# Optimization experiments

Hardware: AMD Instinct MI355X
Metric: run time of the kernel (lower is better)

Reference implementation:

```python
import jax, jax.numpy as jnp
import numpy as np

N = 51200      # total nodes
G = 256        # graphs in batch
NPG = 200      # nodes per graph
E = 409600     # intra-graph edges
EPG = E // G
F_IN, HID, HEADS, NCLS = 768, 128, 4, 2


def setup_inputs() -> dict:
    key = jax.random.key(0)
    ks = jax.random.split(key, 20)
    x = jax.random.normal(ks[0], (N, F_IN), jnp.float32)
    # edges strictly inside each graph, no self-loops (PyG batching semantics)
    gid = jnp.arange(E, dtype=jnp.int32) // EPG
    sl = jax.random.randint(ks[1], (E,), 0, NPG, dtype=jnp.int32)
    off = jax.random.randint(ks[2], (E,), 1, NPG, dtype=jnp.int32)
    dl = (sl + off) % NPG
    edge_index = jnp.stack([gid * NPG + sl, gid * NPG + dl])
    batch = jnp.arange(N, dtype=jnp.int32) // NPG

    def glorot(k, shape, fan_in):
        return jax.random.normal(k, shape, jnp.float32) * np.float32(1.0 / np.sqrt(fan_in))

    return {
        'x': x, 'edge_index': edge_index, 'batch': batch,
        'W1': glorot(ks[3], (F_IN, HEADS * HID), F_IN),
        'a_src1': glorot(ks[4], (HEADS, HID), HID),
        'a_dst1': glorot(ks[5], (HEADS, HID), HID),
        'b1': jnp.zeros((HEADS * HID,), jnp.float32),
        'W2': glorot(ks[6], (HEADS * HID, HID), HEADS * HID),
        'a_src2': glorot(ks[7], (1, HID), HID),
        'a_dst2': glorot(ks[8], (1, HID), HID),
        'b2': jnp.zeros((HID,), jnp.float32),
        'Wc': glorot(ks[9], (HID, 2), HID),
        'bc': jnp.zeros((2,), jnp.float32),
        'Wf1': glorot(ks[10], (HID, HID), HID),
        'bf1': jnp.zeros((HID,), jnp.float32),
        'Wf2': glorot(ks[11], (HID, NCLS), HID),
        'bf2': jnp.zeros((NCLS,), jnp.float32),
    }


def _segment_softmax(logits, seg, num):
    m = jax.ops.segment_max(logits, seg, num_segments=num)
    e = jnp.exp(logits - m[seg])
    s = jax.ops.segment_sum(e, seg, num_segments=num)
    return e / (s[seg] + 1e-16)


def _gat(x, src, dst, W, a_s, a_d, b, n):
    # PyG GATConv, eval mode (attention dropout off), self-loops already in src/dst
    H, C = a_s.shape
    h = (x @ W).reshape(n, H, C)                       # [n,H,C]
    a_src = (h * a_s).sum(-1)                          # [n,H]
    a_dst = (h * a_d).sum(-1)
    logits = jax.nn.leaky_relu(a_src[src] + a_dst[dst], 0.2)  # [Etot,H]
    alpha = _segment_softmax(logits, dst, n)
    out = jax.ops.segment_sum(h[src] * alpha[:, :, None], dst, num_segments=n)
    return out.reshape(n, H * C) + b


def reference(x, edge_index, batch, W1, a_src1, a_dst1, b1, W2, a_src2, a_dst2, b2,
              Wc, bc, Wf1, bf1, Wf2, bf2):
    src0, dst0 = edge_index[0], edge_index[1]
    loop = jnp.arange(N, dtype=src0.dtype)
    src = jnp.concatenate([src0, loop])
    dst = jnp.concatenate([dst0, loop])

    h1 = jax.nn.relu(_gat(x, src, dst, W1, a_src1, a_dst1, b1, N))     # [N,512]
    h2 = jax.nn.relu(_gat(h1, src, dst, W2, a_src2, a_dst2, b2, N))    # [N,128]

    S = jax.nn.softmax(h2 @ Wc + bc, axis=1)                           # [N,2]

    # aggregate(): per-graph S^T A S via per-edge outer products (A from original edges)
    eg = batch[src0]
    outer = S[src0][:, :, None] * S[dst0][:, None, :]                  # [E,2,2]
    agg = jax.ops.segment_sum(outer, eg, num_segments=G)               # [G,2,2]
    rnorm = jnp.clip(jnp.abs(agg).sum(axis=2, keepdims=True), 1e-5, None)  # F.normalize p=1 dim=1
    nadj = agg / rnorm
    diag = jnp.diagonal(nadj, axis1=1, axis2=2)                        # [G,2]
    aggregate_loss = jnp.mean(jnp.mean((diag - 1.0) ** 2, axis=1))     # MSE vs ones, averaged over graphs

    # subgraph embedding: first row of S_g^T x_g per graph
    sub = jax.ops.segment_sum(S[:, 0:1] * h2, batch, num_segments=G)   # [G,128]

    out = jax.nn.relu(sub @ Wf1 + bf1)                                 # eval: dropout off
    out = out @ Wf2 + bf2                                              # [G,2]
    return out, aggregate_loss
```

## Files before the change

kernel.cpp:

```cpp
#include <hip/hip_runtime.h>
#include <hip/hip_bf16.h>
#include <cstdint>

#define N_NODES 51200
#define N_GRAPH 256
#define NPG     200
#define N_EDGE  409600
#define EPG     1600
#define F_IN    768
#define HID     128
#define HEADS   4
#define HC      512

typedef __attribute__((ext_vector_type(8))) short short8;
typedef __attribute__((ext_vector_type(4))) float floatx4;

constexpr size_t OFF_H1B    = 0;
constexpr size_t OFF_H2B    = OFF_H1B + (size_t)N_NODES * HC * 2;
constexpr size_t OFF_H2F    = OFF_H2B + (size_t)N_NODES * HID * 2;
constexpr size_t OFF_WT1    = OFF_H2F + (size_t)N_NODES * HID * 4;
constexpr size_t OFF_WT2    = OFF_WT1 + (size_t)HC * F_IN * 2;
constexpr size_t OFF_S      = OFF_WT2 + (size_t)HID * HC * 2;
constexpr size_t OFF_AGG    = OFF_S + (size_t)N_NODES * 2 * 4;
constexpr size_t OFF_SUB    = OFF_AGG + (size_t)N_GRAPH * 4 * 4;

__device__ __forceinline__ float leaky(float x) { return x >= 0.0f ? x : 0.2f * x; }

__device__ __forceinline__ unsigned short f2bf(float f) {
    unsigned int u = __float_as_uint(f);
    u += 0x7fffu + ((u >> 16) & 1u);
    return (unsigned short)(u >> 16);
}
__device__ __forceinline__ float bflo(int p) { return __uint_as_float((unsigned)p << 16); }
__device__ __forceinline__ float bfhi(int p) { return __uint_as_float((unsigned)p & 0xffff0000u); }

__device__ __forceinline__ unsigned int cvtpk(float lo, float hi) {
    unsigned int r;
    asm("v_cvt_pk_bf16_f32 %0, %1, %2" : "=v"(r) : "v"(lo), "v"(hi));
    return r;
}

__device__ __forceinline__ void gl_lds16(const void* g, void* l) {
    __builtin_amdgcn_global_load_lds(
        (__attribute__((address_space(1))) void*)(g),
        (__attribute__((address_space(3))) void*)(l),
        16, 0, 0);
}

__global__ __launch_bounds__(256)
void transpose_cvt_kernel(const float* __restrict__ W, short* __restrict__ Wt,
                          int K, int Nn)
{
    int idx = blockIdx.x * 256 + threadIdx.x;
    if (idx >= K * Nn) return;
    int k = idx / Nn, n = idx % Nn;
    Wt[(size_t)n * K + k] = (short)f2bf(W[idx]);
}

__global__ __launch_bounds__(256, 3)
void gemm_xw1_kernel(const float* __restrict__ A, const short* __restrict__ Bt,
                     unsigned short* __restrict__ C, int M, int Nn, int K)
{
    __shared__ __align__(16) float Asm[2][128 * 32];
    __shared__ __align__(16) short Bsm[2][4096];
    const int tid = threadIdx.x;
    const int w = tid >> 6, l = tid & 63;

    const int nwg = gridDim.x;
    int wg = blockIdx.x;
    wg = (wg & 7) * (nwg >> 3) + (wg >> 3);
    const int nbx = Nn >> 7;
    const int m0 = (wg / nbx) * 128;
    const int n0 = (wg % nbx) * 128;
    const int wr = w >> 1, wc = w & 1;

    floatx4 acc[4][4];
#pragma unroll
    for (int i = 0; i < 4; ++i)
#pragma unroll
        for (int j = 0; j < 4; ++j) acc[i][j] = (floatx4)0.0f;

    const short* bgp = Bt + (size_t)(n0 + w * 32 + (l & 15)) * K + ((l >> 4) * 8);
    const float* agp = A + (size_t)(m0 + w * 32 + (l & 7)) * K + ((l >> 3) * 4);
    const int nt = K >> 5;

    int aB[4];
#pragma unroll
    for (int mi = 0; mi < 4; ++mi)
        aB[mi] = (wr * 8 + mi * 2 + ((l & 15) >> 3)) * 256 + (l >> 4) * 64 + (l & 7) * 4;
    const int bB0 = wc * 2048 + l * 8;

#define STAGE1(buf, t) {                                                        \
        const int ko_ = (t) * 32;                                               \
        gl_lds16(agp + ko_,              &Asm[buf][w * 1024]);                  \
        gl_lds16(agp + 8 * K + ko_,      &Asm[buf][w * 1024 + 256]);            \
        gl_lds16(agp + 16 * K + ko_,     &Asm[buf][w * 1024 + 512]);            \
        gl_lds16(agp + 24 * K + ko_,     &Asm[buf][w * 1024 + 768]);            \
        gl_lds16(bgp + ko_,              &Bsm[buf][w * 1024]);                  \
        gl_lds16(bgp + 16 * K + ko_,     &Bsm[buf][w * 1024 + 512]); }

#define COMPUTE1(buf) {                                                         \
        short8 af[4], bfr[4];                                                   \
        _Pragma("unroll")                                                       \
        for (int mi = 0; mi < 4; ++mi) {                                        \
            float4 v0 = *(const float4*)&Asm[buf][aB[mi]];                      \
            float4 v1 = *(const float4*)&Asm[buf][aB[mi] + 32];                 \
            uint4 pk;                                                           \
            pk.x = cvtpk(v0.x, v0.y); pk.y = cvtpk(v0.z, v0.w);                 \
            pk.z = cvtpk(v1.x, v1.y); pk.w = cvtpk(v1.z, v1.w);                 \
            af[mi] = *reinterpret_cast<short8*>(&pk);                           \
        }                                                                       \
        _Pragma("unroll")                                                       \
        for (int ni = 0; ni < 4; ++ni)                                          \
            bfr[ni] = *(const short8*)&Bsm[buf][bB0 + ni * 512];                \
        _Pragma("unroll")                                                       \
        for (int mi = 0; mi < 4; ++mi)                                          \
            _Pragma("unroll")                                                   \
            for (int ni = 0; ni < 4; ++ni)                                      \
                acc[mi][ni] = __builtin_amdgcn_mfma_f32_16x16x32_bf16(          \
                    af[mi], bfr[ni], acc[mi][ni], 0, 0, 0); }

    STAGE1(0, 0);
    asm volatile("s_waitcnt vmcnt(0)" ::: "memory");
    __builtin_amdgcn_s_barrier();

    int cur = 0;
    for (int t = 0; t < nt; ++t) {
        if (t + 1 < nt) STAGE1(cur ^ 1, t + 1);
        COMPUTE1(cur);
        if (t + 1 < nt) {
            asm volatile("s_waitcnt vmcnt(0) lgkmcnt(0)" ::: "memory");
            __builtin_amdgcn_s_barrier();
            cur ^= 1;
        }
    }
#undef STAGE1
#undef COMPUTE1

    const int lr = (l >> 4) * 4, lc = l & 15;
#pragma unroll
    for (int mi = 0; mi < 4; ++mi)
#pragma unroll
        for (int ni = 0; ni < 4; ++ni) {
            const size_t base = (size_t)(m0 + wr * 64 + mi * 16 + lr) * Nn
                              + (n0 + wc * 64 + ni * 16 + lc);
#pragma unroll
            for (int rr = 0; rr < 4; ++rr)
                C[base + (size_t)rr * Nn] = f2bf(acc[mi][ni][rr]);
        }
}

__global__ __launch_bounds__(256, 3)
void gemm_bf16_kernel(const short* __restrict__ Ab, const short* __restrict__ Bt,
                      unsigned short* __restrict__ C, int M, int Nn, int K)
{
    __shared__ __align__(16) short Bblob[3][4096];
    __shared__ __align__(16) short Ablob[3][4096];
    const int tid = threadIdx.x;
    const int w = tid >> 6, l = tid & 63;

    const int nwg = gridDim.x;
    int wg = blockIdx.x;
    wg = (wg & 7) * (nwg >> 3) + (wg >> 3);
    const int nbx = Nn >> 7;
    const int m0 = (wg / nbx) * 128;
    const int n0 = (wg % nbx) * 128;
    const int wr = w >> 1, wc = w & 1;
    const int wofs = w * 1024;

    floatx4 acc[4][4];
#pragma unroll
    for (int i = 0; i < 4; ++i)
#pragma unroll
        for (int j = 0; j < 4; ++j) acc[i][j] = (floatx4)0.0f;

    const short* bgp = Bt + (size_t)(n0 + w * 32 + (l & 15)) * K + ((l >> 4) * 8);
    const short* agp = Ab + (size_t)(m0 + w * 32 + (l & 15)) * K + ((l >> 4) * 8);
    const int nt = K >> 5;

    auto compute = [&](int bi) {
        short8 af[4], bfr[4];
#pragma unroll
        for (int mi = 0; mi < 4; ++mi)
            af[mi] = *(const short8*)&Ablob[bi][(wr * 4 + mi) * 512 + l * 8];
#pragma unroll
        for (int ni = 0; ni < 4; ++ni)
            bfr[ni] = *(const short8*)&Bblob[bi][(wc * 4 + ni) * 512 + l * 8];
#pragma unroll
        for (int mi = 0; mi < 4; ++mi)
#pragma unroll
            for (int ni = 0; ni < 4; ++ni)
                acc[mi][ni] = __builtin_amdgcn_mfma_f32_16x16x32_bf16(
                    af[mi], bfr[ni], acc[mi][ni], 0, 0, 0);
    };

    gl_lds16(agp,               &Ablob[0][wofs]);
    gl_lds16(agp + 16 * K,      &Ablob[0][wofs + 512]);
    gl_lds16(bgp,               &Bblob[0][wofs]);
    gl_lds16(bgp + 16 * K,      &Bblob[0][wofs + 512]);
    gl_lds16(agp + 32,          &Ablob[1][wofs]);
    gl_lds16(agp + 16 * K + 32, &Ablob[1][wofs + 512]);
    gl_lds16(bgp + 32,          &Bblob[1][wofs]);
    gl_lds16(bgp + 16 * K + 32, &Bblob[1][wofs + 512]);
    asm volatile("s_waitcnt vmcnt(4)" ::: "memory");
    __builtin_amdgcn_s_barrier();

    int cur3 = 0;
    for (int t = 0; t < nt; ++t) {
        int nn3 = cur3 + 2; if (nn3 >= 3) nn3 -= 3;
        if (t + 2 < nt) {
            const int kk = (t + 2) << 5;
            gl_lds16(agp + kk,          &Ablob[nn3][wofs]);
            gl_lds16(agp + 16 * K + kk, &Ablob[nn3][wofs + 512]);
            gl_lds16(bgp + kk,          &Bblob[nn3][wofs]);
            gl_lds16(bgp + 16 * K + kk, &Bblob[nn3][wofs + 512]);
        }
        compute(cur3);
        if (t + 1 < nt) {
            if (t + 2 < nt) asm volatile("s_waitcnt vmcnt(4) lgkmcnt(0)" ::: "memory");
            else            asm volatile("s_waitcnt vmcnt(0) lgkmcnt(0)" ::: "memory");
            __builtin_amdgcn_s_barrier();
        }
        cur3 += 1; if (cur3 == 3) cur3 = 0;
    }

    const int lr = (l >> 4) * 4, lc = l & 15;
#pragma unroll
    for (int mi = 0; mi < 4; ++mi)
#pragma unroll
        for (int ni = 0; ni < 4; ++ni) {
            const size_t base = (size_t)(m0 + wr * 64 + mi * 16 + lr) * Nn
                              + (n0 + wc * 64 + ni * 16 + lc);
#pragma unroll
            for (int rr = 0; rr < 4; ++rr)
                C[base + (size_t)rr * Nn] = f2bf(acc[mi][ni][rr]);
        }
}

__global__ __launch_bounds__(512)
void gat1_kernel(const unsigned short* __restrict__ H, const int* __restrict__ src0,
                 const int* __restrict__ dst0, const float* __restrict__ a_s,
                 const float* __restrict__ a_d, const float* __restrict__ b1,
                 unsigned short* __restrict__ out)
{
    const int g = blockIdx.x, h = blockIdx.y;
    __shared__ int   s_feat[NPG * 64];
    __shared__ float s_as[NPG], s_ad[NPG], s_m[NPG], s_inv[NPG];
    __shared__ int   s_row[NPG + 1];
    __shared__ int   s_cnt[NPG];
    __shared__ int   s_scan[256];
    __shared__ unsigned short s_eraw[EPG];
    __shared__ int2  s_wc[EPG];
    const int tid = threadIdx.x, w = tid >> 6, l = tid & 63;
    const int gbase = g * NPG;

    for (int flat = tid; flat < NPG * 16; flat += 512) {
        int row = flat >> 4, q = flat & 15;
        uint4 v = *(const uint4*)(H + (size_t)(gbase + row) * HC + h * HID + q * 8);
        *(uint4*)&s_feat[row * 64 + q * 4] = v;
    }
    for (int j = tid; j < EPG; j += 512) {
        int s = src0[g * EPG + j] - gbase;
        int d = dst0[g * EPG + j] - gbase;
        s_eraw[j] = (unsigned short)(s | (d << 8));
    }
    if (tid < NPG) s_cnt[tid] = 0;
    __syncthreads();

    for (int j = tid; j < EPG; j += 512)
        atomicAdd(&s_cnt[s_eraw[j] >> 8], 1);
    const float2 av = ((const float2*)(a_s + h * HID))[l];
    const float2 dv = ((const float2*)(a_d + h * HID))[l];
    for (int nl = w; nl < NPG; nl += 8) {
        int pk = s_feat[nl * 64 + l];
        float f0 = bflo(pk), f1 = bfhi(pk);
        float ss = f0 * av.x + f1 * av.y;
        float sd = f0 * dv.x + f1 * dv.y;
#pragma unroll
        for (int off = 1; off < 64; off <<= 1) {
            ss += __shfl_xor(ss, off);
            sd += __shfl_xor(sd, off);
        }
        if (l == 0) { s_as[nl] = ss; s_ad[nl] = sd; }
    }
    __syncthreads();

    {
        int v = (tid < NPG) ? s_cnt[tid] : 0;
        if (tid < 256) s_scan[tid] = v;
        __syncthreads();
        for (int off = 1; off < 256; off <<= 1) {
            int u = (tid >= off && tid < 256) ? s_scan[tid - off] : 0;
            __syncthreads();
            if (tid < 256) s_scan[tid] += u;
            __syncthreads();
        }
        if (tid < NPG) s_row[tid + 1] = s_scan[tid];
        if (tid == 0) s_row[0] = 0;
        __syncthreads();
        if (tid < NPG) s_scan[tid] = s_row[tid];
    }
    __syncthreads();

    for (int j = tid; j < EPG; j += 512) {
        int pk = s_eraw[j];
        int p = atomicAdd(&s_scan[pk >> 8], 1);
        s_wc[p].y = pk;
    }
    __syncthreads();

    for (int j = tid; j < EPG; j += 512) {
        int pk = s_wc[j].y;
        s_wc[j].x = __float_as_int(leaky(s_as[pk & 255] + s_ad[pk >> 8]));
    }
    __syncthreads();

    if (tid < NPG) {
        float m = leaky(s_as[tid] + s_ad[tid]);
        int r0 = s_row[tid], r1 = s_row[tid + 1];
        for (int j = r0; j < r1; ++j) m = fmaxf(m, __int_as_float(s_wc[j].x));
        s_m[tid] = m;
    }
    __syncthreads();

    for (int j = tid; j < EPG; j += 512) {
        int2 e = s_wc[j];
        s_wc[j].x = __float_as_int(__expf(__int_as_float(e.x) - s_m[e.y >> 8]));
    }
    __syncthreads();

    if (tid < NPG) {
        float rs = __expf(leaky(s_as[tid] + s_ad[tid]) - s_m[tid]);
        int r0 = s_row[tid], r1 = s_row[tid + 1];
        for (int j = r0; j < r1; ++j) rs += __int_as_float(s_wc[j].x);
        s_inv[tid] = 1.0f / (rs + 1e-16f);
    }
    __syncthreads();

    const float2 bv = ((const float2*)(b1 + h * HID))[l];
    for (int nl = w; nl < NPG; nl += 8) {
        const int r0 = s_row[nl], r1 = s_row[nl + 1];
        const float wself = __expf(leaky(s_as[nl] + s_ad[nl]) - s_m[nl]);
        int spk = s_feat[nl * 64 + l];
        float a0 = wself * bflo(spk), a1 = wself * bfhi(spk);
        float c0 = 0.0f, c1 = 0.0f;
        int j = r0;
        for (; j + 4 <= r1; j += 4) {
            int2 e0 = s_wc[j], e1 = s_wc[j + 1], e2 = s_wc[j + 2], e3 = s_wc[j + 3];
            int p0 = s_feat[(e0.y & 255) * 64 + l];
            int p1 = s_feat[(e1.y & 255) * 64 + l];
            int p2 = s_feat[(e2.y & 255) * 64 + l];
            int p3 = s_feat[(e3.y & 255) * 64 + l];
            float w0 = __int_as_float(e0.x), w1 = __int_as_float(e1.x);
            float w2 = __int_as_float(e2.x), w3 = __int_as_float(e3.x);
            a0 += w0 * bflo(p0); a1 += w0 * bfhi(p0);
            c0 += w1 * bflo(p1); c1 += w1 * bfhi(p1);
            a0 += w2 * bflo(p2); a1 += w2 * bfhi(p2);
            c0 += w3 * bflo(p3); c1 += w3 * bfhi(p3);
        }
        for (; j < r1; ++j) {
            int2 e0 = s_wc[j];
            int p0 = s_feat[(e0.y & 255) * 64 + l];
            float w0 = __int_as_float(e0.x);
            a0 += w0 * bflo(p0); a1 += w0 * bfhi(p0);
        }
        const float inv = s_inv[nl];
        float o0 = (a0 + c0) * inv + bv.x;
        float o1 = (a1 + c1) * inv + bv.y;
        unsigned int st = (unsigned int)f2bf(fmaxf(o0, 0.0f))
                        | ((unsigned int)f2bf(fmaxf(o1, 0.0f)) << 16);
        *(unsigned int*)&out[(size_t)(gbase + nl) * HC + h * HID + 2 * l] = st;
    }
}

__global__ __launch_bounds__(512)
void gat2_kernel(const unsigned short* __restrict__ H, const int* __restrict__ src0,
                 const int* __restrict__ dst0, const float* __restrict__ a_s,
                 const float* __restrict__ a_d, const float* __restrict__ b2,
                 const float* __restrict__ Wc, const float* __restrict__ bc,
                 float* __restrict__ sub, float* __restrict__ agg)
{
    const int g = blockIdx.x;
    __shared__ int   s_feat[NPG * 64];
    __shared__ float s_as[NPG], s_ad[NPG], s_m[NPG], s_inv[NPG];
    __shared__ int   s_row[NPG + 1];
    __shared__ int   s_cnt[NPG];
    __shared__ int   s_scan[256];
    __shared__ unsigned short s_eraw[EPG];
    __shared__ int2  s_wc[EPG];
    __shared__ float2 s_Sv[NPG];
    __shared__ float  s_red[8 * 128];
    __shared__ float  s_aggr[8][4];
    const int tid = threadIdx.x, w = tid >> 6, l = tid & 63;
    const int gbase = g * NPG;

    for (int flat = tid; flat < NPG * 16; flat += 512) {
        int row = flat >> 4, q = flat & 15;
        uint4 v = *(const uint4*)(H + (size_t)(gbase + row) * HID + q * 8);
        *(uint4*)&s_feat[row * 64 + q * 4] = v;
    }
    for (int j = tid; j < EPG; j += 512) {
        int s = src0[g * EPG + j] - gbase;
        int d = dst0[g * EPG + j] - gbase;
        s_eraw[j] = (unsigned short)(s | (d << 8));
    }
    if (tid < NPG) s_cnt[tid] = 0;
    __syncthreads();

    for (int j = tid; j < EPG; j += 512)
        atomicAdd(&s_cnt[s_eraw[j] >> 8], 1);
    const float2 av = ((const float2*)a_s)[l];
    const float2 dv = ((const float2*)a_d)[l];
    for (int nl = w; nl < NPG; nl += 8) {
        int pk = s_feat[nl * 64 + l];
        float f0 = bflo(pk), f1 = bfhi(pk);
        float ss = f0 * av.x + f1 * av.y;
        float sd = f0 * dv.x + f1 * dv.y;
#pragma unroll
        for (int off = 1; off < 64; off <<= 1) {
            ss += __shfl_xor(ss, off);
            sd += __shfl_xor(sd, off);
        }
        if (l == 0) { s_as[nl] = ss; s_ad[nl] = sd; }
    }
    __syncthreads();

    {
        int v = (tid < NPG) ? s_cnt[tid] : 0;
        if (tid < 256) s_scan[tid] = v;
        __syncthreads();
        for (int off = 1; off < 256; off <<= 1) {
            int u = (tid >= off && tid < 256) ? s_scan[tid - off] : 0;
            __syncthreads();
            if (tid < 256) s_scan[tid] += u;
            __syncthreads();
        }
        if (tid < NPG) s_row[tid + 1] = s_scan[tid];
        if (tid == 0) s_row[0] = 0;
        __syncthreads();
        if (tid < NPG) s_scan[tid] = s_row[tid];
    }
    __syncthreads();

    for (int j = tid; j < EPG; j += 512) {
        int pk = s_eraw[j];
        int p = atomicAdd(&s_scan[pk >> 8], 1);
        s_wc[p].y = pk;
    }
    __syncthreads();

    for (int j = tid; j < EPG; j += 512) {
        int pk = s_wc[j].y;
        s_wc[j].x = __float_as_int(leaky(s_as[pk & 255] + s_ad[pk >> 8]));
    }
    __syncthreads();

    if (tid < NPG) {
        float m = leaky(s_as[tid] + s_ad[tid]);
        int r0 = s_row[tid], r1 = s_row[tid + 1];
        for (int j = r0; j < r1; ++j) m = fmaxf(m, __int_as_float(s_wc[j].x));
        s_m[tid] = m;
    }
    __syncthreads();

    for (int j = tid; j < EPG; j += 512) {
        int2 e = s_wc[j];
        s_wc[j].x = __float_as_int(__expf(__int_as_float(e.x) - s_m[e.y >> 8]));
    }
    __syncthreads();

    if (tid < NPG) {
        float rs = __expf(leaky(s_as[tid] + s_ad[tid]) - s_m[tid]);
        int r0 = s_row[tid], r1 = s_row[tid + 1];
        for (int j = r0; j < r1; ++j) rs += __int_as_float(s_wc[j].x);
        s_inv[tid] = 1.0f / (rs + 1e-16f);
    }
    __syncthreads();

    const float2 bv = ((const float2*)b2)[l];
    const float4 wcv = ((const float4*)Wc)[l];
    const float bc0 = bc[0], bc1 = bc[1];
    float accs0 = 0.0f, accs1 = 0.0f;
    for (int nl = w; nl < NPG; nl += 8) {
        const int r0 = s_row[nl], r1 = s_row[nl + 1];
        const float wself = __expf(leaky(s_as[nl] + s_ad[nl]) - s_m[nl]);
        int spk = s_feat[nl * 64 + l];
        float a0 = wself * bflo(spk), a1 = wself * bfhi(spk);
        float c0 = 0.0f, c1 = 0.0f;
        int j = r0;
        for (; j + 4 <= r1; j += 4) {
            int2 e0 = s_wc[j], e1 = s_wc[j + 1], e2 = s_wc[j + 2], e3 = s_wc[j + 3];
            int p0 = s_feat[(e0.y & 255) * 64 + l];
            int p1 = s_feat[(e1.y & 255) * 64 + l];
            int p2 = s_feat[(e2.y & 255) * 64 + l];
            int p3 = s_feat[(e3.y & 255) * 64 + l];
            float w0 = __int_as_float(e0.x), w1 = __int_as_float(e1.x);
            float w2 = __int_as_float(e2.x), w3 = __int_as_float(e3.x);
            a0 += w0 * bflo(p0); a1 += w0 * bfhi(p0);
            c0 += w1 * bflo(p1); c1 += w1 * bfhi(p1);
            a0 += w2 * bflo(p2); a1 += w2 * bfhi(p2);
            c0 += w3 * bflo(p3); c1 += w3 * bfhi(p3);
        }
        for (; j < r1; ++j) {
            int2 e0 = s_wc[j];
            int p0 = s_feat[(e0.y & 255) * 64 + l];
            float w0 = __int_as_float(e0.x);
            a0 += w0 * bflo(p0); a1 += w0 * bfhi(p0);
        }
        const float inv = s_inv[nl];
        float o0 = fmaxf((a0 + c0) * inv + bv.x, 0.0f);
        float o1 = fmaxf((a1 + c1) * inv + bv.y, 0.0f);
        float z0 = o0 * wcv.x + o1 * wcv.z;
        float z1 = o0 * wcv.y + o1 * wcv.w;
#pragma unroll
        for (int off = 1; off < 64; off <<= 1) {
            z0 += __shfl_xor(z0, off);
            z1 += __shfl_xor(z1, off);
        }
        z0 += bc0; z1 += bc1;
        float mm = fmaxf(z0, z1);
        float e0 = __expf(z0 - mm), e1 = __expf(z1 - mm);
        float is = 1.0f / (e0 + e1);
        float s0v = e0 * is, s1v = e1 * is;
        if (l == 0) s_Sv[nl] = make_float2(s0v, s1v);
        accs0 += s0v * o0;
        accs1 += s0v * o1;
    }
    s_red[w * 128 + 2 * l]     = accs0;
    s_red[w * 128 + 2 * l + 1] = accs1;
    __syncthreads();

    float a00 = 0, a01 = 0, a10 = 0, a11 = 0;
    for (int j = tid; j < EPG; j += 512) {
        int pk = s_eraw[j];
        float2 Ss = s_Sv[pk & 255];
        float2 Sd = s_Sv[pk >> 8];
        a00 += Ss.x * Sd.x; a01 += Ss.x * Sd.y;
        a10 += Ss.y * Sd.x; a11 += Ss.y * Sd.y;
    }
#pragma unroll
    for (int off = 32; off > 0; off >>= 1) {
        a00 += __shfl_down(a00, off); a01 += __shfl_down(a01, off);
        a10 += __shfl_down(a10, off); a11 += __shfl_down(a11, off);
    }
    if (l == 0) { s_aggr[w][0] = a00; s_aggr[w][1] = a01; s_aggr[w][2] = a10; s_aggr[w][3] = a11; }
    __syncthreads();

    if (tid < 128) {
        float s = 0.0f;
#pragma unroll
        for (int w8 = 0; w8 < 8; ++w8) s += s_red[w8 * 128 + tid];
        sub[(size_t)g * HID + tid] = s;
    }
    if (tid < 4) {
        float s = 0.0f;
#pragma unroll
        for (int w8 = 0; w8 < 8; ++w8) s += s_aggr[w8][tid];
        agg[g * 4 + tid] = s;
    }
}

__global__ __launch_bounds__(256)
void loss_kernel(const float* __restrict__ agg, float* __restrict__ out_loss)
{
    int tid = threadIdx.x;
    float a00 = agg[tid*4 + 0], a01 = agg[tid*4 + 1];
    float a10 = agg[tid*4 + 2], a11 = agg[tid*4 + 3];
    float rn0 = fmaxf(fabsf(a00) + fabsf(a01), 1e-5f);
    float rn1 = fmaxf(fabsf(a10) + fabsf(a11), 1e-5f);
    float d0 = a00 / rn0 - 1.0f, d1 = a11 / rn1 - 1.0f;
    float contrib = 0.5f * (d0*d0 + d1*d1);
    for (int off = 32; off > 0; off >>= 1) contrib += __shfl_down(contrib, off);
    __shared__ float sred[4];
    if ((tid & 63) == 0) sred[tid >> 6] = contrib;
    __syncthreads();
    if (tid == 0)
        out_loss[0] = (sred[0] + sred[1] + sred[2] + sred[3]) * (1.0f / N_GRAPH);
}

__global__ __launch_bounds__(128)
void final_kernel(const float* __restrict__ sub, const float* __restrict__ Wf1,
                  const float* __restrict__ bf1, const float* __restrict__ Wf2,
                  const float* __restrict__ bf2, float* __restrict__ out)
{
    __shared__ float s_sub[128];
    __shared__ float s_fc[128];
    const int g = blockIdx.x, t = threadIdx.x;
    s_sub[t] = sub[g*HID + t];
    __syncthreads();
    float acc = bf1[t];
    for (int c = 0; c < 128; ++c)
        acc += s_sub[c] * Wf1[c*128 + t];
    s_fc[t] = fmaxf(acc, 0.0f);
    __syncthreads();
    if (t < 2) {
        float z = bf2[t];
        for (int j = 0; j < 128; ++j) z += s_fc[j] * Wf2[j*2 + t];
        out[g*2 + t] = z;
    }
}

extern "C" void kernel_launch(void* const* d_in, const int* in_sizes, int n_in,
                              void* d_out, int out_size, void* d_ws, size_t ws_size,
                              hipStream_t stream)
{
    const float* x   = (const float*)d_in[0];
    const int*   ei  = (const int*)d_in[1];
    const float* W1  = (const float*)d_in[3];
    const float* as1 = (const float*)d_in[4];
    const float* ad1 = (const float*)d_in[5];
    const float* b1  = (const float*)d_in[6];
    const float* W2  = (const float*)d_in[7];
    const float* as2 = (const float*)d_in[8];
    const float* ad2 = (const float*)d_in[9];
    const float* b2  = (const float*)d_in[10];
    const float* Wc  = (const float*)d_in[11];
    const float* bc  = (const float*)d_in[12];
    const float* Wf1 = (const float*)d_in[13];
    const float* bf1 = (const float*)d_in[14];
    const float* Wf2 = (const float*)d_in[15];
    const float* bf2 = (const float*)d_in[16];
    const int* src0 = ei;
    const int* dst0 = ei + N_EDGE;

    char* ws = (char*)d_ws;
    unsigned short* H1b = (unsigned short*)(ws + OFF_H1B);
    unsigned short* H2b = (unsigned short*)(ws + OFF_H2B);
    short* Wt1   = (short*)(ws + OFF_WT1);
    short* Wt2   = (short*)(ws + OFF_WT2);
    float* aggb  = (float*)(ws + OFF_AGG);
    float* subb  = (float*)(ws + OFF_SUB);
    float* out   = (float*)d_out;

    transpose_cvt_kernel<<<(F_IN*HC + 255)/256, 256, 0, stream>>>(W1, Wt1, F_IN, HC);
    transpose_cvt_kernel<<<(HC*HID + 255)/256, 256, 0, stream>>>(W2, Wt2, HC, HID);

    gemm_xw1_kernel<<<(N_NODES/128) * (HC/128), 256, 0, stream>>>(
        x, Wt1, H1b, N_NODES, HC, F_IN);

    gat1_kernel<<<dim3(N_GRAPH, HEADS), 512, 0, stream>>>(
        H1b, src0, dst0, as1, ad1, b1, H1b);

    gemm_bf16_kernel<<<(N_NODES/128) * (HID/128), 256, 0, stream>>>(
        (const short*)H1b, Wt2, H2b, N_NODES, HID, HC);

    gat2_kernel<<<N_GRAPH, 512, 0, stream>>>(
        H2b, src0, dst0, as2, ad2, b2, Wc, bc, subb, aggb);

    loss_kernel<<<1, 256, 0, stream>>>(aggb, out + N_GRAPH*2);
    final_kernel<<<N_GRAPH, 128, 0, stream>>>(subb, Wf1, bf1, Wf2, bf2, out);

    (void)in_sizes; (void)n_in; (void)out_size; (void)ws_size;
}
```

Measured before the change: 510.4 us.

## Enlarge XW1 GEMM tile with triple buffering and precompute per-graph CSR once

```diff
diff --git a/kernel.cpp b/kernel.cpp
--- a/kernel.cpp
+++ b/kernel.cpp
@@ -23,6 +23,8 @@
 constexpr size_t OFF_S      = OFF_WT2 + (size_t)HID * HC * 2;
 constexpr size_t OFF_AGG    = OFF_S + (size_t)N_NODES * 2 * 4;
 constexpr size_t OFF_SUB    = OFF_AGG + (size_t)N_GRAPH * 4 * 4;
+constexpr size_t OFF_EORD   = OFF_SUB + (size_t)N_GRAPH * HID * 4;
+constexpr size_t OFF_ROWS   = OFF_EORD + (size_t)N_GRAPH * EPG * 2;
 
 __device__ __forceinline__ float leaky(float x) { return x >= 0.0f ? x : 0.2f * x; }
 
@@ -57,26 +59,26 @@
     Wt[(size_t)n * K + k] = (short)f2bf(W[idx]);
 }
 
-__global__ __launch_bounds__(256, 3)
+__global__ __launch_bounds__(512, 2)
 void gemm_xw1_kernel(const float* __restrict__ A, const short* __restrict__ Bt,
                      unsigned short* __restrict__ C, int M, int Nn, int K)
 {
-    __shared__ __align__(16) float Asm[2][128 * 32];
-    __shared__ __align__(16) short Bsm[2][4096];
+    __shared__ __align__(16) float Asm[3][256 * 32];
+    __shared__ __align__(16) short Bsm[3][256 * 32];
     const int tid = threadIdx.x;
     const int w = tid >> 6, l = tid & 63;
 
     const int nwg = gridDim.x;
     int wg = blockIdx.x;
     wg = (wg & 7) * (nwg >> 3) + (wg >> 3);
-    const int nbx = Nn >> 7;
-    const int m0 = (wg / nbx) * 128;
-    const int n0 = (wg % nbx) * 128;
-    const int wr = w >> 1, wc = w & 1;
-
-    floatx4 acc[4][4];
-#pragma unroll
-    for (int i = 0; i < 4; ++i)
+    const int nbx = Nn >> 8;
+    const int m0 = (wg / nbx) * 256;
+    const int n0 = (wg % nbx) * 256;
+    const int wr = w >> 2, wc = w & 3;
+
+    floatx4 acc[8][4];
+#pragma unroll
+    for (int i = 0; i < 8; ++i)
 #pragma unroll
         for (int j = 0; j < 4; ++j) acc[i][j] = (floatx4)0.0f;
 
@@ -84,65 +86,74 @@
     const float* agp = A + (size_t)(m0 + w * 32 + (l & 7)) * K + ((l >> 3) * 4);
     const int nt = K >> 5;
 
-    int aB[4];
-#pragma unroll
-    for (int mi = 0; mi < 4; ++mi)
-        aB[mi] = (wr * 8 + mi * 2 + ((l & 15) >> 3)) * 256 + (l >> 4) * 64 + (l & 7) * 4;
+    int aB[8];
+#pragma unroll
+    for (int mi = 0; mi < 8; ++mi) {
+        const int r = wr * 128 + mi * 16 + (l & 15);
+        aB[mi] = (r >> 3) * 256 + (l >> 4) * 64 + (r & 7) * 4;
+    }
     const int bB0 = wc * 2048 + l * 8;
 
-#define STAGE1(buf, t) {                                                        \
+#define STAGEX(buf, t) {                                                        \
         const int ko_ = (t) * 32;                                               \
-        gl_lds16(agp + ko_,              &Asm[buf][w * 1024]);                  \
-        gl_lds16(agp + 8 * K + ko_,      &Asm[buf][w * 1024 + 256]);            \
-        gl_lds16(agp + 16 * K + ko_,     &Asm[buf][w * 1024 + 512]);            \
-        gl_lds16(agp + 24 * K + ko_,     &Asm[buf][w * 1024 + 768]);            \
+        gl_lds16(agp + ko_,              &Asm[buf][(w * 4 + 0) * 256]);         \
+        gl_lds16(agp + 8 * K + ko_,      &Asm[buf][(w * 4 + 1) * 256]);         \
+        gl_lds16(agp + 16 * K + ko_,     &Asm[buf][(w * 4 + 2) * 256]);         \
+        gl_lds16(agp + 24 * K + ko_,     &Asm[buf][(w * 4 + 3) * 256]);         \
         gl_lds16(bgp + ko_,              &Bsm[buf][w * 1024]);                  \
         gl_lds16(bgp + 16 * K + ko_,     &Bsm[buf][w * 1024 + 512]); }
 
-#define COMPUTE1(buf) {                                                         \
-        short8 af[4], bfr[4];                                                   \
-        _Pragma("unroll")                                                       \
-        for (int mi = 0; mi < 4; ++mi) {                                        \
-            float4 v0 = *(const float4*)&Asm[buf][aB[mi]];                      \
-            float4 v1 = *(const float4*)&Asm[buf][aB[mi] + 32];                 \
-            uint4 pk;                                                           \
-            pk.x = cvtpk(v0.x, v0.y); pk.y = cvtpk(v0.z, v0.w);                 \
-            pk.z = cvtpk(v1.x, v1.y); pk.w = cvtpk(v1.z, v1.w);                 \
-            af[mi] = *reinterpret_cast<short8*>(&pk);                           \
-        }                                                                       \
+#define COMPUTEX(buf) {                                                         \
+        short8 bfr[4];                                                          \
         _Pragma("unroll")                                                       \
         for (int ni = 0; ni < 4; ++ni)                                          \
             bfr[ni] = *(const short8*)&Bsm[buf][bB0 + ni * 512];                \
         _Pragma("unroll")                                                       \
-        for (int mi = 0; mi < 4; ++mi)                                          \
+        for (int mh = 0; mh < 2; ++mh) {                                        \
+            short8 af[4];                                                       \
             _Pragma("unroll")                                                   \
-            for (int ni = 0; ni < 4; ++ni)                                      \
-                acc[mi][ni] = __builtin_amdgcn_mfma_f32_16x16x32_bf16(          \
-                    af[mi], bfr[ni], acc[mi][ni], 0, 0, 0); }
-
-    STAGE1(0, 0);
-    asm volatile("s_waitcnt vmcnt(0)" ::: "memory");
+            for (int q = 0; q < 4; ++q) {                                       \
+                float4 v0 = *(const float4*)&Asm[buf][aB[mh * 4 + q]];          \
+                float4 v1 = *(const float4*)&Asm[buf][aB[mh * 4 + q] + 32];     \
+                uint4 pk;                                                       \
+                pk.x = cvtpk(v0.x, v0.y); pk.y = cvtpk(v0.z, v0.w);             \
+                pk.z = cvtpk(v1.x, v1.y); pk.w = cvtpk(v1.z, v1.w);             \
+                af[q] = *reinterpret_cast<short8*>(&pk);                        \
+            }                                                                   \
+            _Pragma("unroll")                                                   \
+            for (int q = 0; q < 4; ++q)                                         \
+                _Pragma("unroll")                                               \
+                for (int ni = 0; ni < 4; ++ni)                                  \
+                    acc[mh * 4 + q][ni] = __builtin_amdgcn_mfma_f32_16x16x32_bf16( \
+                        af[q], bfr[ni], acc[mh * 4 + q][ni], 0, 0, 0);          \
+        } }
+
+    STAGEX(0, 0);
+    STAGEX(1, 1);
+    asm volatile("s_waitcnt vmcnt(6)" ::: "memory");
     __builtin_amdgcn_s_barrier();
 
-    int cur = 0;
+    int cur3 = 0;
     for (int t = 0; t < nt; ++t) {
-        if (t + 1 < nt) STAGE1(cur ^ 1, t + 1);
-        COMPUTE1(cur);
+        int nn3 = cur3 + 2; if (nn3 >= 3) nn3 -= 3;
+        if (t + 2 < nt) STAGEX(nn3, t + 2);
+        COMPUTEX(cur3);
         if (t + 1 < nt) {
-            asm volatile("s_waitcnt vmcnt(0) lgkmcnt(0)" ::: "memory");
+            if (t + 2 < nt) asm volatile("s_waitcnt vmcnt(6) lgkmcnt(0)" ::: "memory");
+            else            asm volatile("s_waitcnt vmcnt(0) lgkmcnt(0)" ::: "memory");
             __builtin_amdgcn_s_barrier();
-            cur ^= 1;
-        }
-    }
-#undef STAGE1
-#undef COMPUTE1
+        }
+        cur3 += 1; if (cur3 == 3) cur3 = 0;
+    }
+#undef STAGEX
+#undef COMPUTEX
 
     const int lr = (l >> 4) * 4, lc = l & 15;
 #pragma unroll
-    for (int mi = 0; mi < 4; ++mi)
+    for (int mi = 0; mi < 8; ++mi)
 #pragma unroll
         for (int ni = 0; ni < 4; ++ni) {
-            const size_t base = (size_t)(m0 + wr * 64 + mi * 16 + lr) * Nn
+            const size_t base = (size_t)(m0 + wr * 128 + mi * 16 + lr) * Nn
                               + (n0 + wc * 64 + ni * 16 + lc);
 #pragma unroll
             for (int rr = 0; rr < 4; ++rr)
@@ -150,7 +161,7 @@
         }
 }
 
-__global__ __launch_bounds__(256, 3)
+__global__ __launch_bounds__(256)
 void gemm_bf16_kernel(const short* __restrict__ Ab, const short* __restrict__ Bt,
                       unsigned short* __restrict__ C, int M, int Nn, int K)
 {
@@ -237,19 +248,61 @@
         }
 }
 
+__global__ __launch_bounds__(256)
+void csr_kernel(const int* __restrict__ src0, const int* __restrict__ dst0,
+                unsigned short* __restrict__ eord, int* __restrict__ rows)
+{
+    const int g = blockIdx.x, tid = threadIdx.x;
+    __shared__ unsigned short s_eraw[EPG];
+    __shared__ int s_cnt[NPG];
+    __shared__ int s_scan[256];
+    __shared__ int s_row[NPG + 1];
+    const int gbase = g * NPG;
+
+    if (tid < NPG) s_cnt[tid] = 0;
+    for (int j = tid; j < EPG; j += 256) {
+        int s = src0[g * EPG + j] - gbase;
+        int d = dst0[g * EPG + j] - gbase;
+        s_eraw[j] = (unsigned short)(s | (d << 8));
+    }
+    __syncthreads();
+    for (int j = tid; j < EPG; j += 256)
+        atomicAdd(&s_cnt[s_eraw[j] >> 8], 1);
+    __syncthreads();
+    {
+        int v = (tid < NPG) ? s_cnt[tid] : 0;
+        s_scan[tid] = v;
+        __syncthreads();
+        for (int off = 1; off < 256; off <<= 1) {
+            int u = (tid >= off) ? s_scan[tid - off] : 0;
+            __syncthreads();
+            s_scan[tid] += u;
+            __syncthreads();
+        }
+        if (tid < NPG) s_row[tid + 1] = s_scan[tid];
+        if (tid == 0) s_row[0] = 0;
+        __syncthreads();
+        if (tid < NPG) s_scan[tid] = s_row[tid];
+    }
+    __syncthreads();
+    for (int j = tid; j < EPG; j += 256) {
+        int pk = s_eraw[j];
+        int p = atomicAdd(&s_scan[pk >> 8], 1);
+        eord[(size_t)g * EPG + p] = (unsigned short)pk;
+    }
+    if (tid <= NPG) rows[g * (NPG + 1) + tid] = s_row[tid];
+}
+
 __global__ __launch_bounds__(512)
-void gat1_kernel(const unsigned short* __restrict__ H, const int* __restrict__ src0,
-                 const int* __restrict__ dst0, const float* __restrict__ a_s,
-                 const float* __restrict__ a_d, const float* __restrict__ b1,
-                 unsigned short* __restrict__ out)
+void gat1_kernel(const unsigned short* __restrict__ H,
+                 const unsigned short* __restrict__ eord, const int* __restrict__ rows,
+                 const float* __restrict__ a_s, const float* __restrict__ a_d,
+                 const float* __restrict__ b1, unsigned short* __restrict__ out)
 {
     const int g = blockIdx.x, h = blockIdx.y;
     __shared__ int   s_feat[NPG * 64];
     __shared__ float s_as[NPG], s_ad[NPG], s_m[NPG], s_inv[NPG];
     __shared__ int   s_row[NPG + 1];
-    __shared__ int   s_cnt[NPG];
-    __shared__ int   s_scan[256];
-    __shared__ unsigned short s_eraw[EPG];
     __shared__ int2  s_wc[EPG];
     const int tid = threadIdx.x, w = tid >> 6, l = tid & 63;
     const int gbase = g * NPG;
@@ -259,16 +312,11 @@
         uint4 v = *(const uint4*)(H + (size_t)(gbase + row) * HC + h * HID + q * 8);
         *(uint4*)&s_feat[row * 64 + q * 4] = v;
     }
-    for (int j = tid; j < EPG; j += 512) {
-        int s = src0[g * EPG + j] - gbase;
-        int d = dst0[g * EPG + j] - gbase;
-        s_eraw[j] = (unsigned short)(s | (d << 8));
-    }
-    if (tid < NPG) s_cnt[tid] = 0;
-    __syncthreads();
-
     for (int j = tid; j < EPG; j += 512)
-        atomicAdd(&s_cnt[s_eraw[j] >> 8], 1);
+        s_wc[j].y = eord[(size_t)g * EPG + j];
+    if (tid <= NPG) s_row[tid] = rows[g * (NPG + 1) + tid];
+    __syncthreads();
+
     const float2 av = ((const float2*)(a_s + h * HID))[l];
     const float2 dv = ((const float2*)(a_d + h * HID))[l];
     for (int nl = w; nl < NPG; nl += 8) {
@@ -282,30 +330,6 @@
             sd += __shfl_xor(sd, off);
         }
         if (l == 0) { s_as[nl] = ss; s_ad[nl] = sd; }
-    }
-    __syncthreads();
-
-    {
-        int v = (tid < NPG) ? s_cnt[tid] : 0;
-        if (tid < 256) s_scan[tid] = v;
-        __syncthreads();
-        for (int off = 1; off < 256; off <<= 1) {
-            int u = (tid >= off && tid < 256) ? s_scan[tid - off] : 0;
-            __syncthreads();
-            if (tid < 256) s_scan[tid] += u;
-            __syncthreads();
-        }
-        if (tid < NPG) s_row[tid + 1] = s_scan[tid];
-        if (tid == 0) s_row[0] = 0;
-        __syncthreads();
-        if (tid < NPG) s_scan[tid] = s_row[tid];
-    }
-    __syncthreads();
-
-    for (int j = tid; j < EPG; j += 512) {
-        int pk = s_eraw[j];
-        int p = atomicAdd(&s_scan[pk >> 8], 1);
-        s_wc[p].y = pk;
     }
     __syncthreads();
 
@@ -374,19 +398,17 @@
 }
 
 __global__ __launch_bounds__(512)
-void gat2_kernel(const unsigned short* __restrict__ H, const int* __restrict__ src0,
-                 const int* __restrict__ dst0, const float* __restrict__ a_s,
-                 const float* __restrict__ a_d, const float* __restrict__ b2,
-                 const float* __restrict__ Wc, const float* __restrict__ bc,
+void gat2_kernel(const unsigned short* __restrict__ H,
+                 const unsigned short* __restrict__ eord, const int* __restrict__ rows,
+                 const float* __restrict__ a_s, const float* __restrict__ a_d,
+                 const float* __restrict__ b2, const float* __restrict__ Wc,
+                 const float* __restrict__ bc,
                  float* __restrict__ sub, float* __restrict__ agg)
 {
     const int g = blockIdx.x;
     __shared__ int   s_feat[NPG * 64];
     __shared__ float s_as[NPG], s_ad[NPG], s_m[NPG], s_inv[NPG];
     __shared__ int   s_row[NPG + 1];
-    __shared__ int   s_cnt[NPG];
-    __shared__ int   s_scan[256];
-    __shared__ unsigned short s_eraw[EPG];
     __shared__ int2  s_wc[EPG];
     __shared__ float2 s_Sv[NPG];
     __shared__ float  s_red[8 * 128];
@@ -399,16 +421,11 @@
         uint4 v = *(const uint4*)(H + (size_t)(gbase + row) * HID + q * 8);
         *(uint4*)&s_feat[row * 64 + q * 4] = v;
     }
-    for (int j = tid; j < EPG; j += 512) {
-        int s = src0[g * EPG + j] - gbase;
-        int d = dst0[g * EPG + j] - gbase;
-        s_eraw[j] = (unsigned short)(s | (d << 8));
-    }
-    if (tid < NPG) s_cnt[tid] = 0;
-    __syncthreads();
-
     for (int j = tid; j < EPG; j += 512)
-        atomicAdd(&s_cnt[s_eraw[j] >> 8], 1);
+        s_wc[j].y = eord[(size_t)g * EPG + j];
+    if (tid <= NPG) s_row[tid] = rows[g * (NPG + 1) + tid];
+    __syncthreads();
+
     const float2 av = ((const float2*)a_s)[l];
     const float2 dv = ((const float2*)a_d)[l];
     for (int nl = w; nl < NPG; nl += 8) {
@@ -422,30 +439,6 @@
             sd += __shfl_xor(sd, off);
         }
         if (l == 0) { s_as[nl] = ss; s_ad[nl] = sd; }
-    }
-    __syncthreads();
-
-    {
-        int v = (tid < NPG) ? s_cnt[tid] : 0;
-        if (tid < 256) s_scan[tid] = v;
-        __syncthreads();
-        for (int off = 1; off < 256; off <<= 1) {
-            int u = (tid >= off && tid < 256) ? s_scan[tid - off] : 0;
-            __syncthreads();
-            if (tid < 256) s_scan[tid] += u;
-            __syncthreads();
-        }
-        if (tid < NPG) s_row[tid + 1] = s_scan[tid];
-        if (tid == 0) s_row[0] = 0;
-        __syncthreads();
-        if (tid < NPG) s_scan[tid] = s_row[tid];
-    }
-    __syncthreads();
-
-    for (int j = tid; j < EPG; j += 512) {
-        int pk = s_eraw[j];
-        int p = atomicAdd(&s_scan[pk >> 8], 1);
-        s_wc[p].y = pk;
     }
     __syncthreads();
 
@@ -532,7 +525,7 @@
 
     float a00 = 0, a01 = 0, a10 = 0, a11 = 0;
     for (int j = tid; j < EPG; j += 512) {
-        int pk = s_eraw[j];
+        int pk = s_wc[j].y;
         float2 Ss = s_Sv[pk & 255];
         float2 Sd = s_Sv[pk >> 8];
         a00 += Ss.x * Sd.x; a01 += Ss.x * Sd.y;
@@ -630,22 +623,25 @@
     short* Wt2   = (short*)(ws + OFF_WT2);
     float* aggb  = (float*)(ws + OFF_AGG);
     float* subb  = (float*)(ws + OFF_SUB);
+    unsigned short* eord = (unsigned short*)(ws + OFF_EORD);
+    int*   rowsb = (int*)(ws + OFF_ROWS);
     float* out   = (float*)d_out;
 
     transpose_cvt_kernel<<<(F_IN*HC + 255)/256, 256, 0, stream>>>(W1, Wt1, F_IN, HC);
     transpose_cvt_kernel<<<(HC*HID + 255)/256, 256, 0, stream>>>(W2, Wt2, HC, HID);
-
-    gemm_xw1_kernel<<<(N_NODES/128) * (HC/128), 256, 0, stream>>>(
+    csr_kernel<<<N_GRAPH, 256, 0, stream>>>(src0, dst0, eord, rowsb);
+
+    gemm_xw1_kernel<<<(N_NODES/256) * (HC/256), 512, 0, stream>>>(
         x, Wt1, H1b, N_NODES, HC, F_IN);
 
     gat1_kernel<<<dim3(N_GRAPH, HEADS), 512, 0, stream>>>(
-        H1b, src0, dst0, as1, ad1, b1, H1b);
+        H1b, eord, rowsb, as1, ad1, b1, H1b);
 
     gemm_bf16_kernel<<<(N_NODES/128) * (HID/128), 256, 0, stream>>>(
         (const short*)H1b, Wt2, H2b, N_NODES, HID, HC);
 
     gat2_kernel<<<N_GRAPH, 512, 0, stream>>>(
-        H2b, src0, dst0, as2, ad2, b2, Wc, bc, subb, aggb);
+        H2b, eord, rowsb, as2, ad2, b2, Wc, bc, subb, aggb);
 
     loss_kernel<<<1, 256, 0, stream>>>(aggb, out + N_GRAPH*2);
     final_kernel<<<N_GRAPH, 128, 0, stream>>>(subb, Wf1, bf1, Wf2, bf2, out);
```

Measured after the change: 505.2 us. About the same (-1.0%).
